# Optimization experiments

Hardware: AMD Instinct MI355X
Metric: run time of the kernel (lower is better)

The kernel has to match this reference:

```python
import jax, jax.numpy as jnp
from jax import lax
import numpy as np

B, L, OBS_DIM, ACT_DIM = 4, 1024, 60, 2
D_MODEL, N_LAYERS, D_STATE, D_CONV, EXPAND = 256, 4, 16, 4, 2
D_INNER = EXPAND * D_MODEL
DT_RANK = (D_MODEL + 15) // 16  # mamba_ssm default: ceil(d_model/16)


def setup_inputs() -> dict:
    key = jax.random.key(0)
    ks = jax.random.split(key, 12)
    rn = lambda k, s, sc: jax.random.normal(k, s, jnp.float32) * sc
    return {
        "obs_seq": jax.random.normal(ks[0], (B, L, OBS_DIM), jnp.float32),
        "input_proj_w": rn(ks[1], (D_MODEL, OBS_DIM), OBS_DIM ** -0.5),
        "input_proj_b": jnp.zeros((D_MODEL,), jnp.float32),
        "norm_w": jnp.ones((N_LAYERS, D_MODEL), jnp.float32),
        "norm_b": jnp.zeros((N_LAYERS, D_MODEL), jnp.float32),
        "in_proj_w": rn(ks[2], (N_LAYERS, 2 * D_INNER, D_MODEL), D_MODEL ** -0.5),
        "conv_w": rn(ks[3], (N_LAYERS, D_INNER, D_CONV), D_CONV ** -0.5),
        "conv_b": jnp.zeros((N_LAYERS, D_INNER), jnp.float32),
        "x_proj_w": rn(ks[4], (N_LAYERS, DT_RANK + 2 * D_STATE, D_INNER), D_INNER ** -0.5),
        "dt_proj_w": rn(ks[5], (N_LAYERS, D_INNER, DT_RANK), DT_RANK ** -0.5),
        "dt_proj_b": jnp.full((N_LAYERS, D_INNER), float(np.log(np.expm1(0.01))), jnp.float32),
        "A_log": jnp.log(jnp.broadcast_to(jnp.arange(1, D_STATE + 1, dtype=jnp.float32), (N_LAYERS, D_INNER, D_STATE))),
        "D_skip": jnp.ones((N_LAYERS, D_INNER), jnp.float32),
        "out_proj_w": rn(ks[6], (N_LAYERS, D_MODEL, D_INNER), D_INNER ** -0.5),
        "policy_mean_w": rn(ks[7], (ACT_DIM, D_MODEL), 0.01 * D_MODEL ** -0.5),
        "policy_mean_b": jnp.zeros((ACT_DIM,), jnp.float32),
        "policy_log_std": jnp.zeros((ACT_DIM,), jnp.float32),
        "value_w": rn(ks[8], (1, D_MODEL), D_MODEL ** -0.5),
        "value_b": jnp.zeros((1,), jnp.float32),
    }


def _silu(x):
    return x * jax.nn.sigmoid(x)


def _layer_norm(x, w, b):
    m = jnp.mean(x, -1, keepdims=True)
    v = jnp.mean(jnp.square(x - m), -1, keepdims=True)
    return (x - m) * lax.rsqrt(v + 1e-5) * w + b


def _mamba(x, in_w, cw, cb, xw, dtw, dtb, a_log, d_skip, ow):
    # x: (B, L, d_model)
    xz = jnp.einsum('bld,ed->ble', x, in_w)            # (B, L, 2*d_inner)
    xi, z = xz[..., :D_INNER], xz[..., D_INNER:]
    # depthwise causal conv, width D_CONV
    xp = jnp.pad(xi, ((0, 0), (D_CONV - 1, 0), (0, 0)))
    conv = sum(xp[:, k:k + L, :] * cw[:, k] for k in range(D_CONV)) + cb
    xi = _silu(conv)
    dbc = jnp.einsum('bld,ed->ble', xi, xw)            # (B, L, dt_rank + 2*d_state)
    dt = jax.nn.softplus(jnp.einsum('blr,dr->bld', dbc[..., :DT_RANK], dtw) + dtb)
    Bm = dbc[..., DT_RANK:DT_RANK + D_STATE]           # (B, L, N)
    Cm = dbc[..., DT_RANK + D_STATE:]                  # (B, L, N)
    A = -jnp.exp(a_log)                                # (d_inner, N)
    dA = jnp.exp(dt[..., None] * A)                    # (B, L, d_inner, N)
    dBx = (dt * xi)[..., None] * Bm[:, :, None, :]     # (B, L, d_inner, N)

    def comb(c1, c2):
        a1, b1 = c1
        a2, b2 = c2
        return a2 * a1, a2 * b1 + b2

    _, h = lax.associative_scan(comb, (dA, dBx), axis=1)  # h_t = dA_t*h_{t-1} + dBx_t
    y = jnp.einsum('bldn,bln->bld', h, Cm) + d_skip * xi
    return jnp.einsum('bld,ed->ble', y * _silu(z), ow)


def _forward(obs_seq, input_proj_w, input_proj_b, norm_w, norm_b, in_proj_w, conv_w,
             conv_b, x_proj_w, dt_proj_w, dt_proj_b, A_log, D_skip, out_proj_w,
             policy_mean_w, policy_mean_b, policy_log_std, value_w, value_b):
    x = _silu(jnp.einsum('blo,do->bld', obs_seq, input_proj_w) + input_proj_b)
    for i in range(N_LAYERS):  # pre-norm residual Mamba blocks
        x = x + _mamba(_layer_norm(x, norm_w[i], norm_b[i]), in_proj_w[i], conv_w[i],
                       conv_b[i], x_proj_w[i], dt_proj_w[i], dt_proj_b[i], A_log[i],
                       D_skip[i], out_proj_w[i])
    mu = jnp.einsum('bld,ad->bla', x, policy_mean_w) + policy_mean_b
    std = jnp.broadcast_to(jnp.exp(policy_log_std), mu.shape)
    value = jnp.einsum('bld,od->blo', x, value_w) + value_b
    return mu, std, value


def reference(obs_seq, input_proj_w, input_proj_b, norm_w, norm_b, in_proj_w, conv_w,
              conv_b, x_proj_w, dt_proj_w, dt_proj_b, A_log, D_skip, out_proj_w,
              policy_mean_w, policy_mean_b, policy_log_std, value_w, value_b):
    return _forward(obs_seq, input_proj_w, input_proj_b, norm_w, norm_b, in_proj_w,
                    conv_w, conv_b, x_proj_w, dt_proj_w, dt_proj_b, A_log, D_skip,
                    out_proj_w, policy_mean_w, policy_mean_b, policy_log_std,
                    value_w, value_b)
```

## Files before the change

kernel.cpp:

```cpp
#include <hip/hip_runtime.h>
#include <hip/hip_bf16.h>

#define Bsz 4
#define Lseq 1024
#define OBS 60
#define DM 256
#define DI 512
#define DTR 16
#define DST 16
#define NTOK (Bsz*Lseq)
#define NCH 64
#define CH  16

typedef _Float16 half8 __attribute__((ext_vector_type(8)));
typedef float floatx4 __attribute__((ext_vector_type(4)));

__device__ __forceinline__ float silu_f(float v) {
    return v * (1.f / (1.f + __expf(-v)));
}
__device__ __forceinline__ float softplus_f(float v) {
    return fmaxf(v, 0.f) + log1pf(__expf(-fabsf(v)));
}

__device__ __forceinline__ void compute_dA(float dtv, const float* An,
                                           bool structured, float* dA) {
    if (structured) {
        float p1 = __expf(-dtv);
        float p2 = p1*p1, p4 = p2*p2, p8 = p4*p4;
        dA[0]=p1;      dA[1]=p2;      dA[2]=p2*p1;    dA[3]=p4;
        dA[4]=p4*p1;   dA[5]=p4*p2;   dA[6]=p4*dA[2]; dA[7]=p8;
        dA[8]=p8*p1;   dA[9]=p8*p2;   dA[10]=p8*dA[2];dA[11]=p8*p4;
        dA[12]=p8*dA[4];dA[13]=p8*dA[5];dA[14]=p8*dA[6];dA[15]=p8*p8;
    } else {
        #pragma unroll
        for (int n = 0; n < 16; ++n) dA[n] = __expf(dtv*An[n]);
    }
}

#define NIN_W  (4*1024*256)
#define NX_W   (4*64*512)
#define NOUT_W (4*256*512)
#define NCWT   (4*4*512)
__global__ __launch_bounds__(256) void convert_weights(
    const float* __restrict__ inw, const float* __restrict__ xw,
    const float* __restrict__ ow, const float* __restrict__ cw,
    _Float16* __restrict__ wh_in, _Float16* __restrict__ wh_x,
    _Float16* __restrict__ wh_out, _Float16* __restrict__ cwT) {
    int idx = blockIdx.x*256 + threadIdx.x;
    if (idx < NIN_W) {
        wh_in[idx] = (_Float16)inw[idx];
    } else if (idx < NIN_W + NX_W) {
        int r = idx - NIN_W;
        int layer = r >> 15;
        int rem = r & 32767;
        int n = rem >> 9, k = rem & 511;
        wh_x[r] = (_Float16)((n < 48) ? xw[((size_t)layer*48 + n)*512 + k] : 0.f);
    } else if (idx < NIN_W + NX_W + NOUT_W) {
        int r = idx - NIN_W - NX_W;
        wh_out[r] = (_Float16)ow[r];
    } else if (idx < NIN_W + NX_W + NOUT_W + NCWT) {
        int r = idx - NIN_W - NX_W - NOUT_W;
        int layer = r >> 11;
        int rem = r & 2047;
        int k = rem >> 9, d = rem & 511;
        cwT[r] = (_Float16)cw[layer*2048 + d*4 + k];
    }
}

__global__ __launch_bounds__(256) void input_proj_ln(
    const float* __restrict__ obs, const float* __restrict__ W,
    const float* __restrict__ bias, const float* __restrict__ nw,
    const float* __restrict__ nb, float* __restrict__ x,
    _Float16* __restrict__ xn_h) {
    int t = blockIdx.x; int tid = threadIdx.x;
    __shared__ float so[OBS];
    if (tid < OBS) so[tid] = obs[t*OBS + tid];
    __syncthreads();
    float acc = bias[tid];
    const float* wr = W + tid*OBS;
    #pragma unroll
    for (int k = 0; k < OBS; ++k) acc += so[k]*wr[k];
    float v = silu_f(acc);
    x[t*DM + tid] = v;
    float s = v;
    #pragma unroll
    for (int off = 32; off; off >>= 1) s += __shfl_down(s, off);
    __shared__ float ps[4];
    __shared__ float mean_s, rstd_s;
    int wid = tid >> 6, lane = tid & 63;
    if (lane == 0) ps[wid] = s;
    __syncthreads();
    if (tid == 0) mean_s = (ps[0]+ps[1]+ps[2]+ps[3]) * (1.f/DM);
    __syncthreads();
    float m = mean_s;
    float d = v - m;
    float sq = d*d;
    #pragma unroll
    for (int off = 32; off; off >>= 1) sq += __shfl_down(sq, off);
    if (lane == 0) ps[wid] = sq;
    __syncthreads();
    if (tid == 0) rstd_s = rsqrtf((ps[0]+ps[1]+ps[2]+ps[3])*(1.f/DM) + 1e-5f);
    __syncthreads();
    xn_h[t*DM + tid] = (_Float16)(d * rstd_s * nw[tid] + nb[tid]);
}

template<int BM, int BN, int WM, int WN, int EPI>
__global__ __launch_bounds__(256) void hgemm_nt(
    const _Float16* __restrict__ A, const _Float16* __restrict__ W,
    void* __restrict__ Cout, const float* __restrict__ resid,
    int M, int N, int K, int ldc,
    const float* __restrict__ e0, const float* __restrict__ e1,
    const float* __restrict__ e2, const float* __restrict__ e3,
    const float* __restrict__ e4,
    float* __restrict__ xout, _Float16* __restrict__ xnh) {
    constexpr int MFR = BM/(WM*16);
    constexpr int NFR = BN/(WN*16);
    __shared__ _Float16 As[BM*64];
    __shared__ _Float16 Bs[BN*64];
    int tid = threadIdx.x;
    int r0 = blockIdx.y*BM, c0 = blockIdx.x*BN;
    int w = tid >> 6, lane = tid & 63;
    int wr = w / WN, wc = w % WN;
    floatx4 acc[MFR][NFR];
    #pragma unroll
    for (int i = 0; i < MFR; ++i)
        #pragma unroll
        for (int j = 0; j < NFR; ++j)
            acc[i][j] = (floatx4)0.f;

    for (int k0 = 0; k0 < K; k0 += 64) {
        #pragma unroll
        for (int c = 0; c < BM/32; ++c) {
            int q = tid + 256*c;
            int row = q >> 3, cc = (q & 7)*8;
            half8 v = *(const half8*)&A[(size_t)(r0 + row)*K + k0 + cc];
            *(half8*)&As[row*64 + (cc ^ ((row & 7) << 3))] = v;
        }
        #pragma unroll
        for (int c = 0; c < BN/32; ++c) {
            int q = tid + 256*c;
            int row = q >> 3, cc = (q & 7)*8;
            half8 v = *(const half8*)&W[(size_t)(c0 + row)*K + k0 + cc];
            *(half8*)&Bs[row*64 + (cc ^ ((row & 7) << 3))] = v;
        }
        __syncthreads();
        #pragma unroll
        for (int kc = 0; kc < 2; ++kc) {
            half8 a[MFR], b[NFR];
            int col = kc*32 + (lane >> 4)*8;
            #pragma unroll
            for (int i = 0; i < MFR; ++i) {
                int row = wr*(BM/WM) + i*16 + (lane & 15);
                a[i] = *(const half8*)&As[row*64 + (col ^ ((row & 7) << 3))];
            }
            #pragma unroll
            for (int j = 0; j < NFR; ++j) {
                int row = wc*(BN/WN) + j*16 + (lane & 15);
                b[j] = *(const half8*)&Bs[row*64 + (col ^ ((row & 7) << 3))];
            }
            #pragma unroll
            for (int i = 0; i < MFR; ++i)
                #pragma unroll
                for (int j = 0; j < NFR; ++j)
                    acc[i][j] = __builtin_amdgcn_mfma_f32_16x16x32_f16(a[i], b[j], acc[i][j], 0, 0, 0);
        }
        __syncthreads();
    }
    if constexpr (EPI == 1) {
        _Float16* C = (_Float16*)Cout;
        #pragma unroll
        for (int i = 0; i < MFR; ++i) {
            int m0 = r0 + wr*(BM/WM) + i*16 + (lane >> 4)*4;
            #pragma unroll
            for (int j = 0; j < NFR; ++j) {
                int col = c0 + wc*(BN/WN) + j*16 + (lane & 15);
                #pragma unroll
                for (int t = 0; t < 4; ++t)
                    C[(size_t)(m0 + t)*ldc + col] = (_Float16)acc[i][j][t];
            }
        }
    } else if constexpr (EPI == 2 || EPI == 3) {
        int g = lane >> 4, ln16 = lane & 15;
        #pragma unroll
        for (int t = 0; t < 4; ++t) {
            int row = r0 + wr*16 + g*4 + t;
            #pragma unroll
            for (int j = 0; j < NFR; ++j)
                acc[0][j][t] += resid[(size_t)row*DM + j*16 + ln16];
        }
        if constexpr (EPI == 2) {
            #pragma unroll
            for (int t = 0; t < 4; ++t) {
                int row = r0 + wr*16 + g*4 + t;
                float s = 0.f, sq = 0.f;
                #pragma unroll
                for (int j = 0; j < NFR; ++j) {
                    float v = acc[0][j][t];
                    xout[(size_t)row*DM + j*16 + ln16] = v;
                    s += v; sq += v*v;
                }
                #pragma unroll
                for (int msk = 1; msk < 16; msk <<= 1) {
                    s += __shfl_xor(s, msk);
                    sq += __shfl_xor(sq, msk);
                }
                float mean = s * (1.f/DM);
                float rstd = rsqrtf(sq*(1.f/DM) - mean*mean + 1e-5f);
                #pragma unroll
                for (int j = 0; j < NFR; ++j) {
                    int col = j*16 + ln16;
                    float v = acc[0][j][t];
                    xnh[(size_t)row*DM + col] =
                        (_Float16)((v - mean)*rstd*e0[col] + e1[col]);
                }
            }
        } else {
            float* out = xout;
            #pragma unroll
            for (int t = 0; t < 4; ++t) {
                int row = r0 + wr*16 + g*4 + t;
                float m0 = 0.f, m1 = 0.f, vv = 0.f;
                #pragma unroll
                for (int j = 0; j < NFR; ++j) {
                    int col = j*16 + ln16;
                    float v = acc[0][j][t];
                    m0 += v*e0[col]; m1 += v*e0[DM + col]; vv += v*e3[col];
                }
                #pragma unroll
                for (int msk = 1; msk < 16; msk <<= 1) {
                    m0 += __shfl_xor(m0, msk);
                    m1 += __shfl_xor(m1, msk);
                    vv += __shfl_xor(vv, msk);
                }
                if (ln16 == 0) {
                    out[row*2 + 0] = m0 + e1[0];
                    out[row*2 + 1] = m1 + e1[1];
                    out[2*NTOK + row*2 + 0] = __expf(e2[0]);
                    out[2*NTOK + row*2 + 1] = __expf(e2[1]);
                    out[4*NTOK + row] = vv + e4[0];
                }
            }
        }
    }
}

__global__ __launch_bounds__(256) void xproj_conv_gemm(
    const _Float16* __restrict__ xz_h, const _Float16* __restrict__ Wx,
    const _Float16* __restrict__ cwT, const float* __restrict__ cb,
    float* __restrict__ dbc) {
    __shared__ _Float16 As[32*64];
    __shared__ _Float16 Bs[64*64];
    int tid = threadIdx.x;
    int r0 = blockIdx.x*32;
    int w = tid >> 6, lane = tid & 63;
    int wr = w >> 1, wc = w & 1;
    floatx4 acc[2];
    acc[0] = (floatx4)0.f; acc[1] = (floatx4)0.f;
    for (int k0 = 0; k0 < 512; k0 += 64) {
        {
            int row = tid >> 3, e8 = tid & 7;
            int d = k0 + e8*8;
            int t = r0 + row, l = t & (Lseq-1);
            half8 zero8;
            zero8 = (half8)((_Float16)0.f);
            half8 v0 = (l >= 3) ? *(const half8*)&xz_h[(size_t)(t-3)*1024 + d] : zero8;
            half8 v1 = (l >= 2) ? *(const half8*)&xz_h[(size_t)(t-2)*1024 + d] : zero8;
            half8 v2 = (l >= 1) ? *(const half8*)&xz_h[(size_t)(t-1)*1024 + d] : zero8;
            half8 v3 = *(const half8*)&xz_h[(size_t)t*1024 + d];
            half8 c0 = *(const half8*)&cwT[0*512 + d];
            half8 c1 = *(const half8*)&cwT[1*512 + d];
            half8 c2 = *(const half8*)&cwT[2*512 + d];
            half8 c3 = *(const half8*)&cwT[3*512 + d];
            half8 o;
            #pragma unroll
            for (int e = 0; e < 8; ++e) {
                float a = cb[d + e];
                a += (float)v0[e]*(float)c0[e];
                a += (float)v1[e]*(float)c1[e];
                a += (float)v2[e]*(float)c2[e];
                a += (float)v3[e]*(float)c3[e];
                o[e] = (_Float16)silu_f(a);
            }
            *(half8*)&As[row*64 + ((e8*8) ^ ((row & 7) << 3))] = o;
        }
        #pragma unroll
        for (int c = 0; c < 2; ++c) {
            int q = tid + 256*c;
            int row = q >> 3, cc = (q & 7)*8;
            half8 vv = *(const half8*)&Wx[(size_t)row*512 + k0 + cc];
            *(half8*)&Bs[row*64 + (cc ^ ((row & 7) << 3))] = vv;
        }
        __syncthreads();
        #pragma unroll
        for (int kc = 0; kc < 2; ++kc) {
            int col = kc*32 + (lane >> 4)*8;
            int arow = wr*16 + (lane & 15);
            half8 a = *(const half8*)&As[arow*64 + (col ^ ((arow & 7) << 3))];
            #pragma unroll
            for (int j = 0; j < 2; ++j) {
                int brow = wc*32 + j*16 + (lane & 15);
                half8 b = *(const half8*)&Bs[brow*64 + (col ^ ((brow & 7) << 3))];
                acc[j] = __builtin_amdgcn_mfma_f32_16x16x32_f16(a, b, acc[j], 0, 0, 0);
            }
        }
        __syncthreads();
    }
    int m0 = r0 + wr*16 + (lane >> 4)*4;
    #pragma unroll
    for (int j = 0; j < 2; ++j) {
        int col = wc*32 + j*16 + (lane & 15);
        if (col < 48) {
            #pragma unroll
            for (int t = 0; t < 4; ++t)
                dbc[(size_t)(m0 + t)*48 + col] = acc[j][t];
        }
    }
}

__global__ __launch_bounds__(256) void scan_phaseA(
    const _Float16* __restrict__ xz_h, const float* __restrict__ dbc,
    const float* __restrict__ dtw, const float* __restrict__ dtb,
    const float* __restrict__ a_log, const float* __restrict__ cw,
    const float* __restrict__ cb,
    _Float16* __restrict__ xi_h, _Float16* __restrict__ dt_h,
    _Float16* __restrict__ Ap, _Float16* __restrict__ He) {
    __shared__ float sdbc[CH*48];
    int blk = blockIdx.x;
    int b = blk >> 7; int rem = blk & 127; int c = rem >> 1; int half = rem & 1;
    int d = half*256 + threadIdx.x;
    const float* src = dbc + ((size_t)(b*Lseq + c*CH))*48;
    for (int q = threadIdx.x; q < CH*48; q += 256) sdbc[q] = src[q];
    float wreg[16];
    #pragma unroll
    for (int r = 0; r < DTR; ++r) wreg[r] = dtw[d*DTR + r];
    float bias = dtb[d];
    float4 cwv = *(const float4*)&cw[d*4];
    float cbv = cb[d];
    float An[16];
    bool structured = true;
    #pragma unroll
    for (int n = 0; n < 16; ++n) {
        An[n] = -__expf(a_log[d*16 + n]);
        structured = structured && (fabsf(An[n] + (float)(n+1)) < 1e-4f*(n+1));
    }
    int l0 = c*CH; int t0 = b*Lseq + l0;
    float w0 = 0.f, w1 = 0.f, w2 = 0.f;
    if (l0 >= 3) {
        w0 = (float)xz_h[(size_t)(t0-3)*1024 + d];
        w1 = (float)xz_h[(size_t)(t0-2)*1024 + d];
        w2 = (float)xz_h[(size_t)(t0-1)*1024 + d];
    }
    __syncthreads();
    float h[16] = {};
    float ap[16];
    #pragma unroll
    for (int n = 0; n < 16; ++n) ap[n] = 1.f;
    for (int s = 0; s < CH; ++s) {
        float cur = (float)xz_h[(size_t)(t0+s)*1024 + d];
        float conv = cbv + cwv.x*w0 + cwv.y*w1 + cwv.z*w2 + cwv.w*cur;
        w0 = w1; w1 = w2; w2 = cur;
        float xiv = silu_f(conv);
        float dl = bias;
        #pragma unroll
        for (int r = 0; r < DTR; ++r) dl += sdbc[s*48 + r]*wreg[r];
        float dtv = softplus_f(dl);
        size_t ti = (size_t)(t0+s)*DI + d;
        xi_h[ti] = (_Float16)xiv;
        dt_h[ti] = (_Float16)dtv;
        float u = dtv*xiv;
        float dA[16];
        compute_dA(dtv, An, structured, dA);
        #pragma unroll
        for (int n = 0; n < 16; ++n) {
            h[n] = dA[n]*h[n] + u*sdbc[s*48 + DTR + n];
            ap[n] *= dA[n];
        }
    }
    size_t base = ((size_t)(b*NCH + c)*16)*DI + d;
    #pragma unroll
    for (int n = 0; n < 16; ++n) {
        Ap[base + n*DI] = (_Float16)ap[n];
        He[base + n*DI] = (_Float16)h[n];
    }
}

__global__ __launch_bounds__(256) void scan_phaseB(
    const _Float16* __restrict__ Ap, const _Float16* __restrict__ He,
    _Float16* __restrict__ h0) {
    int g = blockIdx.x*blockDim.x + threadIdx.x;
    int b = g >> 13; int n = (g >> 9) & 15; int d = g & 511;
    float run = 0.f;
    for (int c = 0; c < NCH; ++c) {
        size_t idx = ((size_t)(b*NCH + c)*16 + n)*DI + d;
        float a = (float)Ap[idx], e = (float)He[idx];
        h0[idx] = (_Float16)run;
        run = a*run + e;
    }
}

__global__ __launch_bounds__(256) void scan_phaseC(
    const _Float16* __restrict__ xi_h, const _Float16* __restrict__ dt_h,
    const float* __restrict__ dbc, const float* __restrict__ a_log,
    const float* __restrict__ dskip, const _Float16* __restrict__ xz_h,
    const _Float16* __restrict__ h0, _Float16* __restrict__ yg_h) {
    __shared__ float sdbc[CH*48];
    int blk = blockIdx.x;
    int b = blk >> 7; int rem = blk & 127; int c = rem >> 1; int half = rem & 1;
    int d = half*256 + threadIdx.x;
    const float* src = dbc + ((size_t)(b*Lseq + c*CH))*48;
    for (int q = threadIdx.x; q < CH*48; q += 256) sdbc[q] = src[q];
    float An[16];
    bool structured = true;
    #pragma unroll
    for (int n = 0; n < 16; ++n) {
        An[n] = -__expf(a_log[d*16 + n]);
        structured = structured && (fabsf(An[n] + (float)(n+1)) < 1e-4f*(n+1));
    }
    __syncthreads();
    int t0 = b*Lseq + c*CH;
    float h[16];
    size_t base = ((size_t)(b*NCH + c)*16)*DI + d;
    #pragma unroll
    for (int n = 0; n < 16; ++n) h[n] = (float)h0[base + n*DI];
    float ds = dskip[d];
    for (int s = 0; s < CH; ++s) {
        size_t ti = (size_t)(t0+s)*DI + d;
        float xiv = (float)xi_h[ti];
        float dtv = (float)dt_h[ti];
        float u = dtv*xiv;
        float dA[16];
        compute_dA(dtv, An, structured, dA);
        float y = ds*xiv;
        #pragma unroll
        for (int n = 0; n < 16; ++n) {
            h[n] = dA[n]*h[n] + u*sdbc[s*48 + DTR + n];
            y += h[n]*sdbc[s*48 + DTR + DST + n];
        }
        float zv = (float)xz_h[(size_t)(t0+s)*1024 + DI + d];
        yg_h[ti] = (_Float16)(y * silu_f(zv));
    }
}

extern "C" void kernel_launch(void* const* d_in, const int* in_sizes, int n_in,
                              void* d_out, int out_size, void* d_ws, size_t ws_size,
                              hipStream_t stream) {
    const float* obs = (const float*)d_in[0];
    const float* ipw = (const float*)d_in[1];
    const float* ipb = (const float*)d_in[2];
    const float* nw  = (const float*)d_in[3];
    const float* nb  = (const float*)d_in[4];
    const float* inw = (const float*)d_in[5];
    const float* cw  = (const float*)d_in[6];
    const float* cb  = (const float*)d_in[7];
    const float* xw  = (const float*)d_in[8];
    const float* dtw = (const float*)d_in[9];
    const float* dtb = (const float*)d_in[10];
    const float* alog= (const float*)d_in[11];
    const float* dsk = (const float*)d_in[12];
    const float* ow  = (const float*)d_in[13];
    const float* pw  = (const float*)d_in[14];
    const float* pb  = (const float*)d_in[15];
    const float* ls  = (const float*)d_in[16];
    const float* vw  = (const float*)d_in[17];
    const float* vb  = (const float*)d_in[18];
    float* out = (float*)d_out;

    float* ws = (float*)d_ws;
    float* x   = ws;
    float* dbc = x   + 1048576;
    _Float16* f16b  = (_Float16*)(dbc + 196608);
    _Float16* xz_h  = f16b;
    _Float16* xn_h  = xz_h  + 4194304;
    _Float16* xi_h  = xn_h  + 1048576;
    _Float16* dt_h  = xi_h  + 2097152;
    _Float16* yg_h  = dt_h  + 2097152;
    _Float16* Ap_h  = yg_h  + 2097152;
    _Float16* He_h  = Ap_h  + 2097152;
    _Float16* h0_h  = Ap_h;
    _Float16* wh_in = He_h  + 2097152;
    _Float16* wh_x  = wh_in + 1048576;
    _Float16* wh_out= wh_x  + 131072;
    _Float16* cwT_h = wh_out+ 524288;

    convert_weights<<<(NIN_W + NX_W + NOUT_W + NCWT + 255)/256, 256, 0, stream>>>(
        inw, xw, ow, cw, wh_in, wh_x, wh_out, cwT_h);
    input_proj_ln<<<NTOK, 256, 0, stream>>>(obs, ipw, ipb, nw, nb, x, xn_h);

    for (int i = 0; i < 4; ++i) {
        {
            dim3 g(1024/64, NTOK/128);
            hgemm_nt<128,64,2,2,1><<<g, 256, 0, stream>>>(
                xn_h, wh_in + (size_t)i*1024*256, xz_h, nullptr, NTOK, 1024, 256, 1024,
                nullptr, nullptr, nullptr, nullptr, nullptr, nullptr, nullptr);
        }
        xproj_conv_gemm<<<NTOK/32, 256, 0, stream>>>(
            xz_h, wh_x + (size_t)i*64*512, cwT_h + i*2048, cb + i*DI, dbc);
        scan_phaseA<<<Bsz*NCH*2, 256, 0, stream>>>(
            xz_h, dbc, dtw + (size_t)i*DI*DTR, dtb + i*DI,
            alog + (size_t)i*DI*DST, cw + (size_t)i*DI*4, cb + i*DI,
            xi_h, dt_h, Ap_h, He_h);
        scan_phaseB<<<128, 256, 0, stream>>>(Ap_h, He_h, h0_h);
        scan_phaseC<<<Bsz*NCH*2, 256, 0, stream>>>(
            xi_h, dt_h, dbc, alog + (size_t)i*DI*DST,
            dsk + i*DI, xz_h, h0_h, yg_h);
        {
            dim3 g(1, NTOK/64);
            if (i < 3) {
                hgemm_nt<64,256,4,1,2><<<g, 256, 0, stream>>>(
                    yg_h, wh_out + (size_t)i*256*512, nullptr, x, NTOK, 256, 512, 256,
                    nw + (i+1)*DM, nb + (i+1)*DM, nullptr, nullptr, nullptr, x, xn_h);
            } else {
                hgemm_nt<64,256,4,1,3><<<g, 256, 0, stream>>>(
                    yg_h, wh_out + (size_t)i*256*512, nullptr, x, NTOK, 256, 512, 256,
                    pw, pb, ls, vw, vb, out, nullptr);
            }
        }
    }
}
```

Before: 336.5 us.

## Halve scan chunk length, merge weight conversion with input projection, unroll scan loops

```diff
diff --git a/kernel.cpp b/kernel.cpp
--- a/kernel.cpp
+++ b/kernel.cpp
@@ -9,8 +9,8 @@
 #define DTR 16
 #define DST 16
 #define NTOK (Bsz*Lseq)
-#define NCH 64
-#define CH  16
+#define NCH 128
+#define CH  8
 
 typedef _Float16 half8 __attribute__((ext_vector_type(8)));
 typedef float floatx4 __attribute__((ext_vector_type(4)));
@@ -41,43 +41,48 @@
 #define NX_W   (4*64*512)
 #define NOUT_W (4*256*512)
 #define NCWT   (4*4*512)
-__global__ __launch_bounds__(256) void convert_weights(
+#define NW_TOT (NIN_W + NX_W + NOUT_W + NCWT)
+#define NWB    ((NW_TOT + 255)/256)
+__global__ __launch_bounds__(256) void prep_kernel(
     const float* __restrict__ inw, const float* __restrict__ xw,
     const float* __restrict__ ow, const float* __restrict__ cw,
     _Float16* __restrict__ wh_in, _Float16* __restrict__ wh_x,
-    _Float16* __restrict__ wh_out, _Float16* __restrict__ cwT) {
-    int idx = blockIdx.x*256 + threadIdx.x;
-    if (idx < NIN_W) {
-        wh_in[idx] = (_Float16)inw[idx];
-    } else if (idx < NIN_W + NX_W) {
-        int r = idx - NIN_W;
-        int layer = r >> 15;
-        int rem = r & 32767;
-        int n = rem >> 9, k = rem & 511;
-        wh_x[r] = (_Float16)((n < 48) ? xw[((size_t)layer*48 + n)*512 + k] : 0.f);
-    } else if (idx < NIN_W + NX_W + NOUT_W) {
-        int r = idx - NIN_W - NX_W;
-        wh_out[r] = (_Float16)ow[r];
-    } else if (idx < NIN_W + NX_W + NOUT_W + NCWT) {
-        int r = idx - NIN_W - NX_W - NOUT_W;
-        int layer = r >> 11;
-        int rem = r & 2047;
-        int k = rem >> 9, d = rem & 511;
-        cwT[r] = (_Float16)cw[layer*2048 + d*4 + k];
-    }
-}
-
-__global__ __launch_bounds__(256) void input_proj_ln(
-    const float* __restrict__ obs, const float* __restrict__ W,
-    const float* __restrict__ bias, const float* __restrict__ nw,
+    _Float16* __restrict__ wh_out, _Float16* __restrict__ cwT,
+    const float* __restrict__ obs, const float* __restrict__ ipw,
+    const float* __restrict__ ipb, const float* __restrict__ nw,
     const float* __restrict__ nb, float* __restrict__ x,
     _Float16* __restrict__ xn_h) {
-    int t = blockIdx.x; int tid = threadIdx.x;
     __shared__ float so[OBS];
+    __shared__ float ps[4];
+    __shared__ float mean_s, rstd_s;
+    int tid = threadIdx.x;
+    if (blockIdx.x < NWB) {
+        int idx = blockIdx.x*256 + tid;
+        if (idx < NIN_W) {
+            wh_in[idx] = (_Float16)inw[idx];
+        } else if (idx < NIN_W + NX_W) {
+            int r = idx - NIN_W;
+            int layer = r >> 15;
+            int rem = r & 32767;
+            int n = rem >> 9, k = rem & 511;
+            wh_x[r] = (_Float16)((n < 48) ? xw[((size_t)layer*48 + n)*512 + k] : 0.f);
+        } else if (idx < NIN_W + NX_W + NOUT_W) {
+            int r = idx - NIN_W - NX_W;
+            wh_out[r] = (_Float16)ow[r];
+        } else if (idx < NW_TOT) {
+            int r = idx - NIN_W - NX_W - NOUT_W;
+            int layer = r >> 11;
+            int rem = r & 2047;
+            int k = rem >> 9, d = rem & 511;
+            cwT[r] = (_Float16)cw[layer*2048 + d*4 + k];
+        }
+        return;
+    }
+    int t = blockIdx.x - NWB;
     if (tid < OBS) so[tid] = obs[t*OBS + tid];
     __syncthreads();
-    float acc = bias[tid];
-    const float* wr = W + tid*OBS;
+    float acc = ipb[tid];
+    const float* wr = ipw + tid*OBS;
     #pragma unroll
     for (int k = 0; k < OBS; ++k) acc += so[k]*wr[k];
     float v = silu_f(acc);
@@ -85,8 +90,6 @@
     float s = v;
     #pragma unroll
     for (int off = 32; off; off >>= 1) s += __shfl_down(s, off);
-    __shared__ float ps[4];
-    __shared__ float mean_s, rstd_s;
     int wid = tid >> 6, lane = tid & 63;
     if (lane == 0) ps[wid] = s;
     __syncthreads();
@@ -261,8 +264,7 @@
             int row = tid >> 3, e8 = tid & 7;
             int d = k0 + e8*8;
             int t = r0 + row, l = t & (Lseq-1);
-            half8 zero8;
-            zero8 = (half8)((_Float16)0.f);
+            half8 zero8 = (half8)((_Float16)0.f);
             half8 v0 = (l >= 3) ? *(const half8*)&xz_h[(size_t)(t-3)*1024 + d] : zero8;
             half8 v1 = (l >= 2) ? *(const half8*)&xz_h[(size_t)(t-2)*1024 + d] : zero8;
             half8 v2 = (l >= 1) ? *(const half8*)&xz_h[(size_t)(t-1)*1024 + d] : zero8;
@@ -326,7 +328,7 @@
     _Float16* __restrict__ Ap, _Float16* __restrict__ He) {
     __shared__ float sdbc[CH*48];
     int blk = blockIdx.x;
-    int b = blk >> 7; int rem = blk & 127; int c = rem >> 1; int half = rem & 1;
+    int b = blk >> 8; int rem = blk & 255; int c = rem >> 1; int half = rem & 1;
     int d = half*256 + threadIdx.x;
     const float* src = dbc + ((size_t)(b*Lseq + c*CH))*48;
     for (int q = threadIdx.x; q < CH*48; q += 256) sdbc[q] = src[q];
@@ -355,6 +357,7 @@
     float ap[16];
     #pragma unroll
     for (int n = 0; n < 16; ++n) ap[n] = 1.f;
+    #pragma unroll 4
     for (int s = 0; s < CH; ++s) {
         float cur = (float)xz_h[(size_t)(t0+s)*1024 + d];
         float conv = cbv + cwv.x*w0 + cwv.y*w1 + cwv.z*w2 + cwv.w*cur;
@@ -405,7 +408,7 @@
     const _Float16* __restrict__ h0, _Float16* __restrict__ yg_h) {
     __shared__ float sdbc[CH*48];
     int blk = blockIdx.x;
-    int b = blk >> 7; int rem = blk & 127; int c = rem >> 1; int half = rem & 1;
+    int b = blk >> 8; int rem = blk & 255; int c = rem >> 1; int half = rem & 1;
     int d = half*256 + threadIdx.x;
     const float* src = dbc + ((size_t)(b*Lseq + c*CH))*48;
     for (int q = threadIdx.x; q < CH*48; q += 256) sdbc[q] = src[q];
@@ -423,6 +426,7 @@
     #pragma unroll
     for (int n = 0; n < 16; ++n) h[n] = (float)h0[base + n*DI];
     float ds = dskip[d];
+    #pragma unroll 4
     for (int s = 0; s < CH; ++s) {
         size_t ti = (size_t)(t0+s)*DI + d;
         float xiv = (float)xi_h[ti];
@@ -475,16 +479,16 @@
     _Float16* dt_h  = xi_h  + 2097152;
     _Float16* yg_h  = dt_h  + 2097152;
     _Float16* Ap_h  = yg_h  + 2097152;
-    _Float16* He_h  = Ap_h  + 2097152;
+    _Float16* He_h  = Ap_h  + 4194304;
     _Float16* h0_h  = Ap_h;
-    _Float16* wh_in = He_h  + 2097152;
+    _Float16* wh_in = He_h  + 4194304;
     _Float16* wh_x  = wh_in + 1048576;
     _Float16* wh_out= wh_x  + 131072;
     _Float16* cwT_h = wh_out+ 524288;
 
-    convert_weights<<<(NIN_W + NX_W + NOUT_W + NCWT + 255)/256, 256, 0, stream>>>(
-        inw, xw, ow, cw, wh_in, wh_x, wh_out, cwT_h);
-    input_proj_ln<<<NTOK, 256, 0, stream>>>(obs, ipw, ipb, nw, nb, x, xn_h);
+    prep_kernel<<<NWB + NTOK, 256, 0, stream>>>(
+        inw, xw, ow, cw, wh_in, wh_x, wh_out, cwT_h,
+        obs, ipw, ipb, nw, nb, x, xn_h);
 
     for (int i = 0; i < 4; ++i) {
         {
```

Result: no change. 337.3 us (+0.3%).
